# Kernel tuning notes

Hardware: AMD Instinct MI355X
Metric: run time of the kernel (lower is better)

The kernel has to match this reference:

```python
import jax, jax.numpy as jnp
import numpy as np

B, M, R = 32768, 64, 16

def setup_inputs() -> dict:
    key = jax.random.key(0)
    # x: [B, M, R, 2] real/imag stacked, matching the torch module's input layout
    x = jax.random.normal(key, (B, M, R, 2), dtype=jnp.float32)
    return {"x": x}

def reference(x) -> jnp.ndarray:
    # Combine real/imag channels into a complex matrix per batch element.
    xc = jax.lax.complex(x[..., 0], x[..., 1])  # [B, M, R] complex64
    # Batched reduced QR (replaces the Python loop of per-batch torch.linalg.qr).
    q, _ = jnp.linalg.qr(xc, mode="reduced")    # q: [B, M, R] complex64
    # Split back into stacked real/imag channels: [B, M, R, 2]
    return jnp.stack([q.real, q.imag], axis=-1)
```

## Files before the change

kernel.cpp:

```cpp
#include <hip/hip_runtime.h>


constexpr int Mrows = 64;
constexpr int Rcols = 16;

template <int CTRL, int RM>
__device__ __forceinline__ float dpp_fadd(float v) {
  int s = __builtin_amdgcn_update_dpp(0, __float_as_int(v), CTRL, RM, 0xF, true);
  return v + __int_as_float(s);
}

__device__ __forceinline__ float rdlane(float v, int srclane) {
  return __int_as_float(__builtin_amdgcn_readlane(__float_as_int(v), srclane));
}

__device__ __forceinline__ float wsum64f_fast(float v) {
  v = dpp_fadd<0xB1, 0xF>(v);
  v = dpp_fadd<0x4E, 0xF>(v);
  v = dpp_fadd<0x141, 0xF>(v);
  v = dpp_fadd<0x140, 0xF>(v);
  v = dpp_fadd<0x142, 0xA>(v);
  v = dpp_fadd<0x143, 0xC>(v);
  return rdlane(v, 63);
}

template <int CTRL, int RM>
__device__ __forceinline__ double dpp_dadd(double v) {
  union { double d; int i[2]; } u, s;
  u.d = v;
  s.i[0] = __builtin_amdgcn_update_dpp(0, u.i[0], CTRL, RM, 0xF, true);
  s.i[1] = __builtin_amdgcn_update_dpp(0, u.i[1], CTRL, RM, 0xF, true);
  return v + s.d;
}

__device__ __forceinline__ double rdlaned(double v, int srclane) {
  union { double d; int i[2]; } u, r;
  u.d = v;
  r.i[0] = __builtin_amdgcn_readlane(u.i[0], srclane);
  r.i[1] = __builtin_amdgcn_readlane(u.i[1], srclane);
  return r.d;
}

__device__ __forceinline__ double wsum64d_fast(double v) {
  v = dpp_dadd<0xB1, 0xF>(v);
  v = dpp_dadd<0x4E, 0xF>(v);
  v = dpp_dadd<0x141, 0xF>(v);
  v = dpp_dadd<0x140, 0xF>(v);
  v = dpp_dadd<0x142, 0xA>(v);
  v = dpp_dadd<0x143, 0xC>(v);
  return rdlaned(v, 63);
}

__device__ void qr_f64_fused(const float* __restrict__ x,
                             float* __restrict__ out, int b, int lane) {
  const float4* xp = reinterpret_cast<const float4*>(
      x + (size_t)b * (Mrows * Rcols * 2) + (size_t)lane * (Rcols * 2));
  double xr[Rcols], xi[Rcols], ar[Rcols], ai[Rcols];
#pragma unroll
  for (int k = 0; k < Rcols / 2; ++k) {
    float4 t = xp[k];
    xr[2 * k] = (double)t.x;      xi[2 * k] = (double)t.y;
    xr[2 * k + 1] = (double)t.z;  xi[2 * k + 1] = (double)t.w;
  }
#pragma unroll
  for (int j = 0; j < Rcols; ++j) { ar[j] = xr[j]; ai[j] = xi[j]; }

#pragma unroll
  for (int i = 0; i < Rcols; ++i) {
    double cr = ar[i], ci = ai[i];
    double sq = (lane > i) ? (cr * cr + ci * ci) : 0.0;
    double xnorm2 = wsum64d_fast(sq);
    double alphr = rdlaned(cr, i);
    double alphi = rdlaned(ci, i);

    double tr, ti;
    if (xnorm2 == 0.0 && alphi == 0.0) {
      tr = 0.0;  ti = 0.0;
    } else {
      double nrm = sqrt(alphr * alphr + alphi * alphi + xnorm2);
      double beta = (alphr >= 0.0) ? -nrm : nrm;
      double rb = 1.0 / beta;
      tr = (beta - alphr) * rb;
      ti = -alphi * rb;
      double dr = alphr - beta, di = alphi;
      double inv = 1.0 / (dr * dr + di * di);
      double sr = dr * inv, si = -di * inv;
      if (lane > i) {
        double nr = cr * sr - ci * si;
        double ni = cr * si + ci * sr;
        ar[i] = nr;
        ai[i] = ni;
      }
      if (lane == i) { ar[i] = beta; ai[i] = 0.0; }
    }

    double vr = (lane == i) ? 1.0 : ((lane > i) ? ar[i] : 0.0);
    double vi = (lane == i) ? 0.0 : ((lane > i) ? ai[i] : 0.0);
    const double ctr = tr, cti = -ti;
#pragma unroll
    for (int j = i + 1; j < Rcols; ++j) {
      double pr = fma(vr, ar[j], vi * ai[j]);
      double pi = fma(vr, ai[j], -(vi * ar[j]));
      pr = wsum64d_fast(pr);
      pi = wsum64d_fast(pi);
      double wr = fma(ctr, pr, -(cti * pi));
      double wi = fma(ctr, pi, cti * pr);
      ar[j] = fma(-wr, vr, fma(wi, vi, ar[j]));
      ai[j] = fma(-wr, vi, fma(-wi, vr, ai[j]));
    }

    double swr = xr[i], swi = xi[i];
#pragma unroll
    for (int k = 0; k < Rcols; ++k) {
      if (k >= i) break;
      double rr = rdlaned(ar[i], k);
      double ri = rdlaned(ai[i], k);
      swr = fma(-xr[k], rr, fma(xi[k], ri, swr));
      swi = fma(-xr[k], ri, fma(-xi[k], rr, swi));
    }
    double rbd = 1.0 / rdlaned(ar[i], i);
    xr[i] = swr * rbd;
    xi[i] = swi * rbd;
  }

  float4* op = reinterpret_cast<float4*>(
      out + (size_t)b * (Mrows * Rcols * 2) + (size_t)lane * (Rcols * 2));
#pragma unroll
  for (int k = 0; k < Rcols / 2; ++k) {
    op[k] = make_float4((float)xr[2 * k], (float)xi[2 * k],
                        (float)xr[2 * k + 1], (float)xi[2 * k + 1]);
  }
}

__global__ __launch_bounds__(256)
__attribute__((amdgpu_waves_per_eu(3)))
void qr_fused(const float* __restrict__ x, float* __restrict__ out, int B) {
  const int lane = threadIdx.x & 63;
  const int wave = threadIdx.x >> 6;
  const int b = blockIdx.x * 4 + wave;
  if (b >= B) return;

  const float4* xp = reinterpret_cast<const float4*>(
      x + (size_t)b * (Mrows * Rcols * 2) + (size_t)lane * (Rcols * 2));
  float xr[Rcols], xi[Rcols];
  float ar[Rcols], ai[Rcols];
#pragma unroll
  for (int k = 0; k < Rcols / 2; ++k) {
    float4 t = xp[k];
    xr[2 * k] = t.x;  xi[2 * k] = t.y;
    xr[2 * k + 1] = t.z;  xi[2 * k + 1] = t.w;
  }
#pragma unroll
  for (int j = 0; j < Rcols; ++j) { ar[j] = xr[j]; ai[j] = xi[j]; }

  bool risky = false;

#pragma unroll
  for (int i = 0; i < Rcols; ++i) {
    float cr = ar[i], ci = ai[i];
    float sq = (lane > i) ? fmaf(cr, cr, ci * ci) : 0.0f;
    float xnorm2 = wsum64f_fast(sq);
    float alphr = rdlane(cr, i);
    float alphi = rdlane(ci, i);

    risky = risky || (fabsf(alphr) < 2e-4f);

    float tr, ti;
    if (xnorm2 == 0.0f && alphi == 0.0f) {
      tr = 0.0f;  ti = 0.0f;
    } else {
      float nrm = __builtin_amdgcn_sqrtf(
          fmaf(alphr, alphr, fmaf(alphi, alphi, xnorm2)));
      float beta = (alphr >= 0.0f) ? -nrm : nrm;
      float rb = __builtin_amdgcn_rcpf(beta);
      tr = (beta - alphr) * rb;
      ti = -alphi * rb;
      float dr = alphr - beta, di = alphi;
      float inv = __builtin_amdgcn_rcpf(fmaf(dr, dr, di * di));
      float sr = dr * inv, si = -di * inv;
      if (lane > i) {
        float nr = fmaf(cr, sr, -(ci * si));
        float ni = fmaf(cr, si, ci * sr);
        ar[i] = nr;
        ai[i] = ni;
      }
      if (lane == i) { ar[i] = beta; ai[i] = 0.0f; }
    }

    float vr = (lane == i) ? 1.0f : ((lane > i) ? ar[i] : 0.0f);
    float vi = (lane == i) ? 0.0f : ((lane > i) ? ai[i] : 0.0f);
    const float ctr = tr, cti = -ti;
#pragma unroll
    for (int j = i + 1; j < Rcols; ++j) {
      float pr = fmaf(vr, ar[j], vi * ai[j]);
      float pi = fmaf(vr, ai[j], -(vi * ar[j]));
      pr = wsum64f_fast(pr);
      pi = wsum64f_fast(pi);
      float wr = fmaf(ctr, pr, -(cti * pi));
      float wi = fmaf(ctr, pi, cti * pr);
      ar[j] = fmaf(-wr, vr, fmaf(wi, vi, ar[j]));
      ai[j] = fmaf(-wr, vi, fmaf(-wi, vr, ai[j]));
    }

    float swr = xr[i], swi = xi[i];
#pragma unroll
    for (int k = 0; k < Rcols; ++k) {
      if (k >= i) break;
      float rr = rdlane(ar[i], k);
      float ri = rdlane(ai[i], k);
      swr = fmaf(-xr[k], rr, fmaf(xi[k], ri, swr));
      swi = fmaf(-xr[k], ri, fmaf(-xi[k], rr, swi));
    }
    float rb = __builtin_amdgcn_rcpf(rdlane(ar[i], i));
    xr[i] = swr * rb;
    xi[i] = swi * rb;
  }

  if (risky) {
    qr_f64_fused(x, out, b, lane);
    return;
  }

  float4* op = reinterpret_cast<float4*>(
      out + (size_t)b * (Mrows * Rcols * 2) + (size_t)lane * (Rcols * 2));
#pragma unroll
  for (int k = 0; k < Rcols / 2; ++k) {
    op[k] = make_float4(xr[2 * k], xi[2 * k], xr[2 * k + 1], xi[2 * k + 1]);
  }
}

extern "C" void kernel_launch(void* const* d_in, const int* in_sizes, int n_in,
                              void* d_out, int out_size, void* d_ws,
                              size_t ws_size, hipStream_t stream) {
  const float* x = (const float*)d_in[0];
  float* out = (float*)d_out;
  const int B = in_sizes[0] / (Mrows * Rcols * 2);
  dim3 block(256);
  dim3 grid((B + 3) / 4);
  qr_fused<<<grid, block, 0, stream>>>(x, out, B);
}
```

Before: 640.2 us.

## Redistribute matrix so each lane owns one column of 16 rows for Householder QR

Changes the data layout of the fp32 path so lane c of each 16-lane group holds column c for 16 rows, instead of one row per lane. Column dot products become local FMAs plus two cross-row permlane swap reductions, replacing a full-wave DPP reduction per column. The Q back-solve now runs as a rank-1 update on a separate P copy, using ds_swizzle/bpermute broadcasts. This cuts cross-lane reduction latency per step, at the cost of more registers (four 16-element arrays plus temporaries) and extra swizzle traffic.

New measurement: 585.6 us. -8.5%, faster.

```diff
diff --git a/kernel.cpp b/kernel.cpp
--- a/kernel.cpp
+++ b/kernel.cpp
@@ -4,24 +4,46 @@
 constexpr int Mrows = 64;
 constexpr int Rcols = 16;
 
-template <int CTRL, int RM>
-__device__ __forceinline__ float dpp_fadd(float v) {
-  int s = __builtin_amdgcn_update_dpp(0, __float_as_int(v), CTRL, RM, 0xF, true);
-  return v + __int_as_float(s);
-}
+typedef int v2i __attribute__((ext_vector_type(2)));
+
+#if defined(__has_builtin)
+#if __has_builtin(__builtin_amdgcn_permlane16_swap)
+#define USE_PL16 1
+#else
+#define USE_PL16 0
+#endif
+#if __has_builtin(__builtin_amdgcn_permlane32_swap)
+#define USE_PL32 1
+#else
+#define USE_PL32 0
+#endif
+#else
+#define USE_PL16 0
+#define USE_PL32 0
+#endif
 
 __device__ __forceinline__ float rdlane(float v, int srclane) {
   return __int_as_float(__builtin_amdgcn_readlane(__float_as_int(v), srclane));
 }
 
-__device__ __forceinline__ float wsum64f_fast(float v) {
-  v = dpp_fadd<0xB1, 0xF>(v);
-  v = dpp_fadd<0x4E, 0xF>(v);
-  v = dpp_fadd<0x141, 0xF>(v);
-  v = dpp_fadd<0x140, 0xF>(v);
-  v = dpp_fadd<0x142, 0xA>(v);
-  v = dpp_fadd<0x143, 0xC>(v);
-  return rdlane(v, 63);
+__device__ __forceinline__ float plswap16_addf(float v) {
+#if USE_PL16
+  v2i r = __builtin_amdgcn_permlane16_swap(__float_as_int(v), __float_as_int(v),
+                                           false, false);
+  return __int_as_float(r[0]) + __int_as_float(r[1]);
+#else
+  return v + __shfl_xor(v, 16, 64);
+#endif
+}
+
+__device__ __forceinline__ float plswap32_addf(float v) {
+#if USE_PL32
+  v2i r = __builtin_amdgcn_permlane32_swap(__float_as_int(v), __float_as_int(v),
+                                           false, false);
+  return __int_as_float(r[0]) + __int_as_float(r[1]);
+#else
+  return v + __shfl_xor(v, 32, 64);
+#endif
 }
 
 template <int CTRL, int RM>
@@ -132,6 +154,108 @@
   }
 }
 
+template <int I>
+__device__ __forceinline__ void qr_step(int lane, float (&Ar)[16], float (&Ai)[16],
+                                        float (&Pr)[16], float (&Pi)[16],
+                                        int bpaR, bool& risky) {
+  const int c = lane & 15;
+  const bool g0 = (lane < 16);
+
+  float ahi = 0.f, alo = 0.f;
+#pragma unroll
+  for (int m = 0; m < 16; ++m) {
+    float s = fmaf(Ar[m], Ar[m], Ai[m] * Ai[m]);
+    if (m > I) ahi += s; else alo += s;
+  }
+  float locn = g0 ? ahi : (ahi + alo);
+  locn = plswap16_addf(locn);
+  locn = plswap32_addf(locn);
+  float xnorm2 = rdlane(locn, I);
+  float alphr = rdlane(Ar[I], I);
+  float alphi = rdlane(Ai[I], I);
+  risky = risky || (fabsf(alphr) < 2e-4f);
+
+  float ctr, cti, dr, di, beta_s;
+  if (xnorm2 == 0.f && alphi == 0.f) {
+    ctr = 0.f; cti = 0.f; dr = 0.f; di = 0.f;
+    beta_s = alphr;
+  } else {
+    float nrm = __builtin_amdgcn_sqrtf(
+        fmaf(alphr, alphr, fmaf(alphi, alphi, xnorm2)));
+    float beta = (alphr >= 0.f) ? -nrm : nrm;
+    float rbeta = __builtin_amdgcn_rcpf(beta);
+    float tr = (beta - alphr) * rbeta;
+    float ti = -alphi * rbeta;
+    dr = alphr - beta;  di = alphi;
+    float inv = __builtin_amdgcn_rcpf(fmaf(dr, dr, di * di));
+    ctr = tr * inv;
+    cti = -(ti * inv);
+    beta_s = beta;
+  }
+  float rbq = __builtin_amdgcn_rcpf(beta_s);
+
+  float ur[16], ui[16];
+#pragma unroll
+  for (int m = 0; m < 16; ++m) {
+    ur[m] = __int_as_float(__builtin_amdgcn_ds_swizzle(
+        __float_as_int(Ar[m]), (I << 5) | 0x10));
+    ui[m] = __int_as_float(__builtin_amdgcn_ds_swizzle(
+        __float_as_int(Ai[m]), (I << 5) | 0x10));
+  }
+#pragma unroll
+  for (int m = 0; m < I; ++m) {
+    ur[m] = g0 ? 0.f : ur[m];
+    ui[m] = g0 ? 0.f : ui[m];
+  }
+  ur[I] = g0 ? dr : ur[I];
+  ui[I] = g0 ? di : ui[I];
+
+  float pr = 0.f, pi = 0.f;
+#pragma unroll
+  for (int m = 0; m < 16; ++m) {
+    pr = fmaf(ur[m], Ar[m], fmaf(ui[m], Ai[m], pr));
+    pi = fmaf(ur[m], Ai[m], fmaf(-ui[m], Ar[m], pi));
+  }
+  pr = plswap16_addf(pr);  pr = plswap32_addf(pr);
+  pi = plswap16_addf(pi);  pi = plswap32_addf(pi);
+  const bool cle = (c <= I);
+  pr = cle ? 0.f : pr;
+  pi = cle ? 0.f : pi;
+
+  float wr = fmaf(ctr, pr, -(cti * pi));
+  float wi = fmaf(ctr, pi, cti * pr);
+#pragma unroll
+  for (int m = 0; m < 16; ++m) {
+    Ar[m] = fmaf(-wr, ur[m], fmaf(wi, ui[m], Ar[m]));
+    Ai[m] = fmaf(-wr, ui[m], fmaf(-wi, ur[m], Ai[m]));
+  }
+
+  float rr = __int_as_float(
+      __builtin_amdgcn_ds_bpermute(bpaR, __float_as_int(Ar[I])));
+  float ri = __int_as_float(
+      __builtin_amdgcn_ds_bpermute(bpaR, __float_as_int(Ai[I])));
+  const bool ceq = (c == I);
+  const bool clt = (c < I);
+  rr = ceq ? (beta_s - 1.f) : rr;
+  rr = clt ? 0.f : rr;
+  ri = cle ? 0.f : ri;
+
+#pragma unroll
+  for (int m = 0; m < 16; ++m) {
+    ur[m] = __int_as_float(__builtin_amdgcn_ds_swizzle(
+        __float_as_int(Pr[m]), (I << 5) | 0x10));
+    ui[m] = __int_as_float(__builtin_amdgcn_ds_swizzle(
+        __float_as_int(Pi[m]), (I << 5) | 0x10));
+  }
+#pragma unroll
+  for (int m = 0; m < 16; ++m) {
+    float qbr = ur[m] * rbq;
+    float qbi = ui[m] * rbq;
+    Pr[m] = fmaf(-qbr, rr, fmaf(qbi, ri, Pr[m]));
+    Pi[m] = fmaf(-qbr, ri, fmaf(-qbi, rr, Pi[m]));
+  }
+}
+
 __global__ __launch_bounds__(256)
 __attribute__((amdgpu_waves_per_eu(3)))
 void qr_fused(const float* __restrict__ x, float* __restrict__ out, int B) {
@@ -139,93 +263,48 @@
   const int wave = threadIdx.x >> 6;
   const int b = blockIdx.x * 4 + wave;
   if (b >= B) return;
-
-  const float4* xp = reinterpret_cast<const float4*>(
-      x + (size_t)b * (Mrows * Rcols * 2) + (size_t)lane * (Rcols * 2));
-  float xr[Rcols], xi[Rcols];
-  float ar[Rcols], ai[Rcols];
-#pragma unroll
-  for (int k = 0; k < Rcols / 2; ++k) {
-    float4 t = xp[k];
-    xr[2 * k] = t.x;  xi[2 * k] = t.y;
-    xr[2 * k + 1] = t.z;  xi[2 * k + 1] = t.w;
-  }
-#pragma unroll
-  for (int j = 0; j < Rcols; ++j) { ar[j] = xr[j]; ai[j] = xi[j]; }
+  const int c = lane & 15;
+  const int gbase = lane & 48;
+  const int bpaR = c << 2;
+
+  const float2* xp = reinterpret_cast<const float2*>(x) +
+                     (size_t)b * (Mrows * Rcols) + (size_t)gbase * Rcols + c;
+  float Ar[16], Ai[16], Pr[16], Pi[16];
+#pragma unroll
+  for (int m = 0; m < 16; ++m) {
+    float2 t = xp[m * Rcols];
+    Ar[m] = t.x;  Ai[m] = t.y;
+    Pr[m] = t.x;  Pi[m] = t.y;
+  }
 
   bool risky = false;
-
-#pragma unroll
-  for (int i = 0; i < Rcols; ++i) {
-    float cr = ar[i], ci = ai[i];
-    float sq = (lane > i) ? fmaf(cr, cr, ci * ci) : 0.0f;
-    float xnorm2 = wsum64f_fast(sq);
-    float alphr = rdlane(cr, i);
-    float alphi = rdlane(ci, i);
-
-    risky = risky || (fabsf(alphr) < 2e-4f);
-
-    float tr, ti;
-    if (xnorm2 == 0.0f && alphi == 0.0f) {
-      tr = 0.0f;  ti = 0.0f;
-    } else {
-      float nrm = __builtin_amdgcn_sqrtf(
-          fmaf(alphr, alphr, fmaf(alphi, alphi, xnorm2)));
-      float beta = (alphr >= 0.0f) ? -nrm : nrm;
-      float rb = __builtin_amdgcn_rcpf(beta);
-      tr = (beta - alphr) * rb;
-      ti = -alphi * rb;
-      float dr = alphr - beta, di = alphi;
-      float inv = __builtin_amdgcn_rcpf(fmaf(dr, dr, di * di));
-      float sr = dr * inv, si = -di * inv;
-      if (lane > i) {
-        float nr = fmaf(cr, sr, -(ci * si));
-        float ni = fmaf(cr, si, ci * sr);
-        ar[i] = nr;
-        ai[i] = ni;
-      }
-      if (lane == i) { ar[i] = beta; ai[i] = 0.0f; }
-    }
-
-    float vr = (lane == i) ? 1.0f : ((lane > i) ? ar[i] : 0.0f);
-    float vi = (lane == i) ? 0.0f : ((lane > i) ? ai[i] : 0.0f);
-    const float ctr = tr, cti = -ti;
-#pragma unroll
-    for (int j = i + 1; j < Rcols; ++j) {
-      float pr = fmaf(vr, ar[j], vi * ai[j]);
-      float pi = fmaf(vr, ai[j], -(vi * ar[j]));
-      pr = wsum64f_fast(pr);
-      pi = wsum64f_fast(pi);
-      float wr = fmaf(ctr, pr, -(cti * pi));
-      float wi = fmaf(ctr, pi, cti * pr);
-      ar[j] = fmaf(-wr, vr, fmaf(wi, vi, ar[j]));
-      ai[j] = fmaf(-wr, vi, fmaf(-wi, vr, ai[j]));
-    }
-
-    float swr = xr[i], swi = xi[i];
-#pragma unroll
-    for (int k = 0; k < Rcols; ++k) {
-      if (k >= i) break;
-      float rr = rdlane(ar[i], k);
-      float ri = rdlane(ai[i], k);
-      swr = fmaf(-xr[k], rr, fmaf(xi[k], ri, swr));
-      swi = fmaf(-xr[k], ri, fmaf(-xi[k], rr, swi));
-    }
-    float rb = __builtin_amdgcn_rcpf(rdlane(ar[i], i));
-    xr[i] = swr * rb;
-    xi[i] = swi * rb;
-  }
+  qr_step<0>(lane, Ar, Ai, Pr, Pi, bpaR, risky);
+  qr_step<1>(lane, Ar, Ai, Pr, Pi, bpaR, risky);
+  qr_step<2>(lane, Ar, Ai, Pr, Pi, bpaR, risky);
+  qr_step<3>(lane, Ar, Ai, Pr, Pi, bpaR, risky);
+  qr_step<4>(lane, Ar, Ai, Pr, Pi, bpaR, risky);
+  qr_step<5>(lane, Ar, Ai, Pr, Pi, bpaR, risky);
+  qr_step<6>(lane, Ar, Ai, Pr, Pi, bpaR, risky);
+  qr_step<7>(lane, Ar, Ai, Pr, Pi, bpaR, risky);
+  qr_step<8>(lane, Ar, Ai, Pr, Pi, bpaR, risky);
+  qr_step<9>(lane, Ar, Ai, Pr, Pi, bpaR, risky);
+  qr_step<10>(lane, Ar, Ai, Pr, Pi, bpaR, risky);
+  qr_step<11>(lane, Ar, Ai, Pr, Pi, bpaR, risky);
+  qr_step<12>(lane, Ar, Ai, Pr, Pi, bpaR, risky);
+  qr_step<13>(lane, Ar, Ai, Pr, Pi, bpaR, risky);
+  qr_step<14>(lane, Ar, Ai, Pr, Pi, bpaR, risky);
+  qr_step<15>(lane, Ar, Ai, Pr, Pi, bpaR, risky);
 
   if (risky) {
     qr_f64_fused(x, out, b, lane);
     return;
   }
 
-  float4* op = reinterpret_cast<float4*>(
-      out + (size_t)b * (Mrows * Rcols * 2) + (size_t)lane * (Rcols * 2));
-#pragma unroll
-  for (int k = 0; k < Rcols / 2; ++k) {
-    op[k] = make_float4(xr[2 * k], xi[2 * k], xr[2 * k + 1], xi[2 * k + 1]);
+  float2* op = reinterpret_cast<float2*>(out) +
+               (size_t)b * (Mrows * Rcols) + (size_t)gbase * Rcols + c;
+#pragma unroll
+  for (int m = 0; m < 16; ++m) {
+    op[m * Rcols] = make_float2(Pr[m], Pi[m]);
   }
 }
 
```
